# Kernel optimization log

Measured on AMD Instinct MI355X. Metric: run time of the kernel, lower is better.

Reference implementation:

```python
import jax, jax.numpy as jnp
import numpy as np
from jax import lax

WS = (8, 7, 7)
NUM_HEADS = 8
KEY_DIM = 16
D = 32  # attn_ratio * key_dim == dim // num_heads
DIM = 256
B = 128
EPS = 1e-5
SCALE = KEY_DIM ** -0.5


def _rel_index():
    d, h, w = WS
    coords = np.stack(np.meshgrid(np.arange(d), np.arange(h), np.arange(w), indexing='ij'))  # [3,d,h,w]
    cf = coords.reshape(3, -1)
    rc = (cf[:, :, None] - cf[:, None, :]).transpose(1, 2, 0)  # [N,N,3]
    rc[..., 0] += d - 1
    rc[..., 1] += h - 1
    rc[..., 2] += w - 1
    rc[..., 0] *= (2 * h - 1) * (2 * w - 1)
    rc[..., 1] *= 2 * w - 1
    return rc.sum(-1).astype(np.int32)  # [N,N]


def setup_inputs() -> dict:
    key = jax.random.key(0)
    ks = jax.random.split(key, 20)
    table = (2 * WS[0] - 1) * (2 * WS[1] - 1) * (2 * WS[2] - 1)  # 2535
    f32 = jnp.float32
    inp = {
        'x': jax.random.normal(ks[0], (B, DIM) + WS, f32),
        'qkv_w': jax.random.normal(ks[1], (NUM_HEADS, 2 * KEY_DIM + D, DIM // NUM_HEADS), f32) * 0.1,
        'qkv_g': 0.5 + 0.5 * jax.random.uniform(ks[2], (NUM_HEADS, 2 * KEY_DIM + D), f32),
        'qkv_b': jax.random.normal(ks[3], (NUM_HEADS, 2 * KEY_DIM + D), f32) * 0.1,
        'qkv_m': jax.random.normal(ks[4], (NUM_HEADS, 2 * KEY_DIM + D), f32) * 0.1,
        'qkv_v': 0.5 + jax.random.uniform(ks[5], (NUM_HEADS, 2 * KEY_DIM + D), f32),
        'dw_w': jax.random.normal(ks[6], (NUM_HEADS, KEY_DIM, 1, 3, 3, 3), f32) * 0.1,
        'dw_g': 0.5 + 0.5 * jax.random.uniform(ks[7], (NUM_HEADS, KEY_DIM), f32),
        'dw_b': jax.random.normal(ks[8], (NUM_HEADS, KEY_DIM), f32) * 0.1,
        'dw_m': jax.random.normal(ks[9], (NUM_HEADS, KEY_DIM), f32) * 0.1,
        'dw_v': 0.5 + jax.random.uniform(ks[10], (NUM_HEADS, KEY_DIM), f32),
        'proj_w': jax.random.normal(ks[11], (DIM, D * NUM_HEADS), f32) * 0.05,
        'proj_g': 0.5 + 0.5 * jax.random.uniform(ks[12], (DIM,), f32),
        'proj_b': jax.random.normal(ks[13], (DIM,), f32) * 0.1,
        'proj_m': jax.random.normal(ks[14], (DIM,), f32) * 0.1,
        'proj_v': 0.5 + jax.random.uniform(ks[15], (DIM,), f32),
        'rpb': jax.random.normal(ks[16], (table, NUM_HEADS), f32) * 0.02,
        'rel_index': jnp.asarray(_rel_index()),
    }
    return inp


def _bn(x, g, b, m, v):
    # x: [B, C, N], inference-form batchnorm over channel axis 1
    s = g / jnp.sqrt(v + EPS)
    return x * s[None, :, None] + (b - m * s)[None, :, None]


def reference(x, qkv_w, qkv_g, qkv_b, qkv_m, qkv_v, dw_w, dw_g, dw_b, dw_m, dw_v,
              proj_w, proj_g, proj_b, proj_m, proj_v, rpb, rel_index):
    Bsz, C, Wd, Wh, Ww = x.shape
    N = Wd * Wh * Ww
    nh = qkv_w.shape[0]
    # relative position bias: [nh, N, N]
    bias = rpb[rel_index.reshape(-1)].reshape(N, N, nh).transpose(2, 0, 1)
    feats_in = jnp.split(x.reshape(Bsz, C, N), nh, axis=1)  # nh x [B, C/nh, N]
    feats_out = []
    feat = feats_in[0]
    for i in range(nh):
        if i > 0:
            feat = feat + feats_in[i]
        # 1x1x1 conv + BN
        h = jnp.einsum('oi,bin->bon', qkv_w[i], feat)
        h = _bn(h, qkv_g[i], qkv_b[i], qkv_m[i], qkv_v[i])
        q, k, v = jnp.split(h, [KEY_DIM, 2 * KEY_DIM], axis=1)  # [B,kd,N],[B,kd,N],[B,d,N]
        # depthwise 3x3x3 conv on q + BN
        q3 = q.reshape(Bsz, KEY_DIM, Wd, Wh, Ww)
        q3 = lax.conv_general_dilated(q3, dw_w[i], window_strides=(1, 1, 1),
                                      padding=((1, 1), (1, 1), (1, 1)),
                                      feature_group_count=KEY_DIM,
                                      dimension_numbers=('NCDHW', 'OIDHW', 'NCDHW'))
        q = _bn(q3.reshape(Bsz, KEY_DIM, N), dw_g[i], dw_b[i], dw_m[i], dw_v[i])
        # attention over the N window tokens
        attn = jnp.einsum('bcn,bcm->bnm', q, k) * SCALE + bias[i]
        attn = jax.nn.softmax(attn, axis=-1)
        feat = jnp.einsum('bcm,bnm->bcn', v, attn)  # v @ attn^T -> [B, d, N]
        feats_out.append(feat)
    cat = jnp.concatenate(feats_out, axis=1)  # [B, d*nh, N]
    out = jnp.einsum('oi,bin->bon', proj_w, jax.nn.relu(cat))
    out = _bn(out, proj_g, proj_b, proj_m, proj_v)
    return out.reshape(Bsz, C, Wd, Wh, Ww)
```

## Files before the change

kernel.cpp:

```cpp
#include <hip/hip_runtime.h>
#include <hip/hip_bf16.h>
#include <cstdint>
#include <cstddef>


#define NH    8
#define KD    16
#define DV    32
#define CH    32
#define QKVO  64
#define DIMC  256
#define NTOK  392
#define NPAD  448
#define BSZ   128
#define EPSV  1e-5f
#define SCL2  0.3606737602222409f
#define LOG2E 1.4426950408889634f
#define MQ    98

typedef float f32x4 __attribute__((ext_vector_type(4)));
typedef short bf16x8 __attribute__((ext_vector_type(8)));
typedef unsigned int u32x4 __attribute__((ext_vector_type(4)));
typedef unsigned int u32x2 __attribute__((ext_vector_type(2)));

__device__ inline unsigned rne_bf16_bits(float x) {
  unsigned u = __float_as_uint(x);
  return (u + 0x7fffu + ((u >> 16) & 1u)) >> 16;
}
__device__ inline unsigned cvt_pk(float a, float b) {
  unsigned r;
  asm("v_cvt_pk_bf16_f32 %0, %1, %2" : "=v"(r) : "v"(a), "v"(b));
  return r;
}
__device__ inline float b2f_lo(unsigned w) { return __uint_as_float(w << 16); }
__device__ inline float b2f_hi(unsigned w) { return __uint_as_float(w & 0xffff0000u); }

__global__ __launch_bounds__(256) void k_biasM(const float* __restrict__ rpb,
                                               const int* __restrict__ rel,
                                               float* __restrict__ biasM) {
  int idx = blockIdx.x * 256 + threadIdx.x;
  if (idx >= NH * MQ * NTOK * 4) return;
  int j = idx & 3;
  int r1 = idx >> 2;
  int n = r1 % NTOK;
  int r2 = r1 / NTOK;
  int mq = r2 % MQ;
  int h = r2 / MQ;
  int m = min(4 * mq + j, NTOK - 1);
  biasM[idx] = rpb[rel[n * NTOK + m] * NH + h] * LOG2E;
}

__global__ __launch_bounds__(256) void k_wsplit(const float* __restrict__ W,
                                                short* __restrict__ Whi,
                                                short* __restrict__ Wlo) {
  int i = blockIdx.x * 256 + threadIdx.x;
  if (i >= DIMC * DIMC) return;
  float v = W[i];
  unsigned u = __float_as_uint(v) & 0xffff0000u;
  Whi[i] = (short)(u >> 16);
  Wlo[i] = (short)rne_bf16_bits(v - __uint_as_float(u));
}
__global__ __launch_bounds__(256) void k_wsplitq(const float* __restrict__ W,
                                                 short* __restrict__ Whi,
                                                 short* __restrict__ Wlo) {
  int i = blockIdx.x * 256 + threadIdx.x;
  if (i >= NH * QKVO * CH) return;
  float v = W[i];
  unsigned u = __float_as_uint(v) & 0xffff0000u;
  Whi[i] = (short)(u >> 16);
  Wlo[i] = (short)rne_bf16_bits(v - __uint_as_float(u));
}

__global__ __launch_bounds__(256) void k_qkv0(
    const float* __restrict__ x, const float* __restrict__ W,
    const float* __restrict__ G, const float* __restrict__ Bp,
    const float* __restrict__ Mp, const float* __restrict__ Vp,
    float* __restrict__ qb0, short* __restrict__ kT0, short* __restrict__ vb0,
    short* __restrict__ kT1, short* __restrict__ vb1) {
  int t = threadIdx.x;
  int b = blockIdx.y;
  int n = blockIdx.x * 64 + (t & 63);
  int w = t >> 6;
  int o0 = __builtin_amdgcn_readfirstlane(w * 16);
  int nc = min(n, NTOK - 1);

  const float* xp = x + (size_t)b * DIMC * NTOK + nc;
  float f[CH];
#pragma unroll
  for (int c = 0; c < CH; ++c) f[c] = xp[(size_t)c * NTOK];

  float acc[16];
#pragma unroll
  for (int oi = 0; oi < 16; ++oi) acc[oi] = 0.f;
#pragma unroll
  for (int c = 0; c < CH; ++c) {
    float fv = f[c];
#pragma unroll
    for (int oi = 0; oi < 16; ++oi) acc[oi] += W[(o0 + oi) * CH + c] * fv;
  }
  float r[16];
#pragma unroll
  for (int oi = 0; oi < 16; ++oi) {
    int o = o0 + oi;
    float s = G[o] * rsqrtf(Vp[o] + EPSV);
    float sh = Bp[o] - Mp[o] * s;
    r[oi] = acc[oi] * s + sh;
  }

  if (w == 0) {
    if (n < NTOK) {
#pragma unroll
      for (int oi = 0; oi < 16; ++oi)
        qb0[((size_t)b * KD + oi) * NTOK + n] = r[oi];
    }
  } else if (w == 1) {
    unsigned wh[8], wl[8];
#pragma unroll
    for (int i = 0; i < 8; ++i) wh[i] = cvt_pk(r[2 * i], r[2 * i + 1]);
#pragma unroll
    for (int i = 0; i < 8; ++i)
      wl[i] = cvt_pk(r[2 * i] - b2f_lo(wh[i]), r[2 * i + 1] - b2f_hi(wh[i]));
    short* row = kT0 + ((size_t)b * NPAD + n) * 32;
    *(u32x4*)&row[0]  = (u32x4){wh[0], wh[1], wh[2], wh[3]};
    *(u32x4*)&row[8]  = (u32x4){wh[4], wh[5], wh[6], wh[7]};
    *(u32x4*)&row[16] = (u32x4){wl[0], wl[1], wl[2], wl[3]};
    *(u32x4*)&row[24] = (u32x4){wl[4], wl[5], wl[6], wl[7]};
    if (n >= NTOK) {
      short* row1 = kT1 + ((size_t)b * NPAD + n) * 32;
#pragma unroll
      for (int p = 0; p < 4; ++p) *(u32x4*)&row1[p * 8] = (u32x4){0, 0, 0, 0};
    }
  } else {
    int vc0 = (w - 2) * 16;
#pragma unroll
    for (int oi = 0; oi < 16; ++oi)
      vb0[((size_t)b * DV + vc0 + oi) * NPAD + n] = (short)rne_bf16_bits(r[oi]);
    if (n >= NTOK) {
#pragma unroll
      for (int oi = 0; oi < 16; ++oi)
        vb1[((size_t)b * DV + vc0 + oi) * NPAD + n] = 0;
    }
  }
}

__global__ __launch_bounds__(256, 8) void k_head(int head,
    const float* __restrict__ x,
    const float* __restrict__ qbC, const short* __restrict__ kTC,
    const short* __restrict__ vbC, const float* __restrict__ biasM,
    const float* __restrict__ DW, const float* __restrict__ dG,
    const float* __restrict__ dB, const float* __restrict__ dM,
    const float* __restrict__ dV,
    const short* __restrict__ Wqhi, const short* __restrict__ Wqlo,
    const float* __restrict__ qG, const float* __restrict__ qBp,
    const float* __restrict__ qM, const float* __restrict__ qV,
    unsigned* __restrict__ catB, float* __restrict__ qbN,
    short* __restrict__ kTN, short* __restrict__ vbN) {
  __shared__ float wdw[432];
  __shared__ float qstage[16][17];
  __shared__ __align__(16) float ubuf[2304];
  __shared__ float lM[4][16];
  __shared__ float oF[32][17];
  __shared__ float xs[32][17];

  int t = threadIdx.x;
  int id = blockIdx.x;
  int r8 = id & 7;
  int jd = id >> 3;
  int qt = jd % 25;
  int b = 8 * (jd / 25) + r8;
  int w = t >> 6, l = t & 63;
  int ln = l & 15, g = l >> 4;
  int tok16 = t & 15, gr = t >> 4;
  int koff = ((g >> 1) << 4) + ((g & 1) << 3);

  {
    float (*hs)[132] = (float(*)[132])ubuf;
    for (int i = t; i < 432; i += 256) wdw[i] = DW[head * 432 + i];
    const float* qpb = qbC + (size_t)b * KD * NTOK;
    int nlo = qt * 16 - 57;
    for (int i = t; i < 16 * 130; i += 256) {
      int c = i / 130, r = i - c * 130;
      int n = nlo + r;
      hs[c][r] = (n >= 0 && n < NTOK) ? qpb[(size_t)c * NTOK + n] : 0.f;
    }
    __syncthreads();
    int tokg = qt * 16 + tok16;
    int tkc = min(tokg, NTOK - 1);
    int z = tkc / 49, rm = tkc - z * 49, y = rm / 7, xx = rm - y * 7;
    const float* wt = &wdw[gr * 27];
    float a = 0.f;
#pragma unroll
    for (int dz = 0; dz < 3; ++dz) {
      int zz = z + dz - 1;
      if (zz < 0 || zz >= 8) continue;
#pragma unroll
      for (int dy = 0; dy < 3; ++dy) {
        int yy = y + dy - 1;
        if (yy < 0 || yy >= 7) continue;
#pragma unroll
        for (int dx = 0; dx < 3; ++dx) {
          int xw = xx + dx - 1;
          if (xw < 0 || xw >= 7) continue;
          a += wt[dz * 9 + dy * 3 + dx] * hs[gr][zz * 49 + yy * 7 + xw - nlo];
        }
      }
    }
    float s = dG[head * KD + gr] * rsqrtf(dV[head * KD + gr] + EPSV);
    float sh = dB[head * KD + gr] - dM[head * KD + gr] * s;
    __syncthreads();
    qstage[gr][tok16] = (a * s + sh) * SCL2;
  }
  __syncthreads();

  bf16x8 qB1, qB2;
  {
    float qv[8];
#pragma unroll
    for (int j2 = 0; j2 < 8; ++j2) qv[j2] = qstage[8 * (g & 1) + j2][ln];
    u32x4 hw;
#pragma unroll
    for (int i = 0; i < 4; ++i) hw[i] = cvt_pk(qv[2 * i], qv[2 * i + 1]);
    qB1 = *(bf16x8*)&hw;
    if (g < 2) {
      u32x4 lw;
#pragma unroll
      for (int i = 0; i < 4; ++i)
        lw[i] = cvt_pk(qv[2 * i] - b2f_lo(hw[i]), qv[2 * i + 1] - b2f_hi(hw[i]));
      qB2 = *(bf16x8*)&lw;
    } else {
#pragma unroll
      for (int j2 = 0; j2 < 8; ++j2) qB2[j2] = 0;
    }
  }

  int tokq = qt * 16 + ln;
  int tqc = min(tokq, NTOK - 1);
  const short* kbase = kTC + (size_t)b * NPAD * 32;
  const short* vbase = vbC + (size_t)b * DV * NPAD;
  const float* bb = biasM + ((size_t)head * MQ * NTOK + tqc) * 4;
  unsigned* pb = (unsigned*)ubuf + w * 576;

  f32x4 oacc[2];
#pragma unroll
  for (int ct = 0; ct < 2; ++ct) oacc[ct] = (f32x4){0.f, 0.f, 0.f, 0.f};
  float lsum = 0.f;

  for (int mt = w; mt < 7; mt += 4) {
    int m0 = mt * 64;
    bf16x8 aK[4];
#pragma unroll
    for (int ms = 0; ms < 4; ++ms)
      aK[ms] = *(const bf16x8*)&kbase[(size_t)(m0 + 16 * ms + ln) * 32 + koff];
    f32x4 bv[4];
#pragma unroll
    for (int ms = 0; ms < 4; ++ms) {
      int mq = min((m0 + 16 * ms + 4 * g) >> 2, MQ - 1);
      bv[ms] = *(const f32x4*)&bb[(size_t)mq * (NTOK * 4)];
    }
    bf16x8 aV[4];
#pragma unroll
    for (int ch = 0; ch < 2; ++ch)
#pragma unroll
      for (int ct = 0; ct < 2; ++ct)
        aV[ch * 2 + ct] = *(const bf16x8*)&vbase[(size_t)(16 * ct + ln) * NPAD
                                                 + m0 + 32 * ch + 8 * g];
    f32x4 S[4];
#pragma unroll
    for (int ms = 0; ms < 4; ++ms) {
      f32x4 a = __builtin_amdgcn_mfma_f32_16x16x32_bf16(aK[ms], qB1, bv[ms], 0, 0, 0);
      S[ms] = __builtin_amdgcn_mfma_f32_16x16x32_bf16(aK[ms], qB2, a, 0, 0, 0);
    }
#pragma unroll
    for (int ms = 0; ms < 4; ++ms) {
      int mk = m0 + 16 * ms + 4 * g;
      float p[4];
#pragma unroll
      for (int r = 0; r < 4; ++r) {
        float sv = fminf(S[ms][r], 96.f);
        if (mk + r >= NTOK) sv = -1e30f;
        p[r] = __builtin_amdgcn_exp2f(sv);
        lsum += p[r];
      }
      u32x2 pw = (u32x2){cvt_pk(p[0], p[1]), cvt_pk(p[2], p[3])};
      *(u32x2*)&pb[ln * 36 + 8 * ms + 2 * g] = pw;
    }
#pragma unroll
    for (int ch = 0; ch < 2; ++ch) {
      u32x4 pk4 = *(const u32x4*)&pb[ln * 36 + 16 * ch + 4 * g];
      bf16x8 pf = *(bf16x8*)&pk4;
#pragma unroll
      for (int ct = 0; ct < 2; ++ct)
        oacc[ct] = __builtin_amdgcn_mfma_f32_16x16x32_bf16(aV[ch * 2 + ct], pf, oacc[ct], 0, 0, 0);
    }
  }

  __syncthreads();
  float (*oP)[32][17] = (float(*)[32][17])ubuf;
  lsum += __shfl_xor(lsum, 16);
  lsum += __shfl_xor(lsum, 32);
#pragma unroll
  for (int ct = 0; ct < 2; ++ct)
#pragma unroll
    for (int r = 0; r < 4; ++r) oP[w][16 * ct + 4 * g + r][ln] = oacc[ct][r];
  if (g == 0) lM[w][ln] = lsum;
  __syncthreads();

  {
    int tokg = qt * 16 + tok16;
    float lt = lM[0][tok16] + lM[1][tok16] + lM[2][tok16] + lM[3][tok16];
    float inv = 1.f / fmaxf(lt, 1e-30f);
    int c0 = 2 * gr, c1 = c0 + 1;
    float a0 = (oP[0][c0][tok16] + oP[1][c0][tok16] + oP[2][c0][tok16] + oP[3][c0][tok16]) * inv;
    float a1 = (oP[0][c1][tok16] + oP[1][c1][tok16] + oP[2][c1][tok16] + oP[3][c1][tok16]) * inv;
    oF[c0][tok16] = a0;
    oF[c1][tok16] = a1;
    if (tokg < NTOK)
      catB[((size_t)b * 128 + head * 16 + gr) * NTOK + tokg] =
          cvt_pk(fmaxf(a0, 0.f), fmaxf(a1, 0.f));
    if (head < 7) {
      for (int i = t; i < 512; i += 256) {
        int c = i >> 4, tk = i & 15;
        int tg = min(qt * 16 + tk, NTOK - 1);
        xs[c][tk] = x[((size_t)b * DIMC + (head + 1) * CH + c) * NTOK + tg];
      }
    }
  }
  __syncthreads();

  if (head < 7) {
    const short* wqh = Wqhi + ((size_t)(head + 1) * QKVO + 16 * w + ln) * CH + 8 * g;
    const short* wql = Wqlo + ((size_t)(head + 1) * QKVO + 16 * w + ln) * CH + 8 * g;
    bf16x8 Ah = *(const bf16x8*)wqh;
    bf16x8 Al = *(const bf16x8*)wql;
    float f8[8];
#pragma unroll
    for (int j2 = 0; j2 < 8; ++j2) f8[j2] = oF[8 * g + j2][ln] + xs[8 * g + j2][ln];
    u32x4 bh, blw;
#pragma unroll
    for (int i = 0; i < 4; ++i) {
      bh[i] = cvt_pk(f8[2 * i], f8[2 * i + 1]);
      blw[i] = cvt_pk(f8[2 * i] - b2f_lo(bh[i]), f8[2 * i + 1] - b2f_hi(bh[i]));
    }
    bf16x8 Bh = *(bf16x8*)&bh;
    bf16x8 Bl = *(bf16x8*)&blw;
    f32x4 acc = (f32x4){0.f, 0.f, 0.f, 0.f};
    acc = __builtin_amdgcn_mfma_f32_16x16x32_bf16(Ah, Bh, acc, 0, 0, 0);
    acc = __builtin_amdgcn_mfma_f32_16x16x32_bf16(Ah, Bl, acc, 0, 0, 0);
    acc = __builtin_amdgcn_mfma_f32_16x16x32_bf16(Al, Bh, acc, 0, 0, 0);
    float r4[4];
#pragma unroll
    for (int r = 0; r < 4; ++r) {
      int o = 16 * w + 4 * g + r;
      int idx = (head + 1) * QKVO + o;
      float s = qG[idx] * rsqrtf(qV[idx] + EPSV);
      float sh = qBp[idx] - qM[idx] * s;
      r4[r] = acc[r] * s + sh;
    }
    int tokg = qt * 16 + ln;
    if (tokg < NTOK) {
      if (w == 0) {
#pragma unroll
        for (int r = 0; r < 4; ++r)
          qbN[((size_t)b * KD + 4 * g + r) * NTOK + tokg] = r4[r];
      } else if (w == 1) {
        unsigned h0 = cvt_pk(r4[0], r4[1]), h1 = cvt_pk(r4[2], r4[3]);
        unsigned l0 = cvt_pk(r4[0] - b2f_lo(h0), r4[1] - b2f_hi(h0));
        unsigned l1 = cvt_pk(r4[2] - b2f_lo(h1), r4[3] - b2f_hi(h1));
        short* row = kTN + ((size_t)b * NPAD + tokg) * 32;
        *(u32x2*)&row[4 * g]      = (u32x2){h0, h1};
        *(u32x2*)&row[16 + 4 * g] = (u32x2){l0, l1};
      } else {
        int vc0 = 16 * (w - 2) + 4 * g;
#pragma unroll
        for (int r = 0; r < 4; ++r)
          vbN[((size_t)b * DV + vc0 + r) * NPAD + tokg] = (short)rne_bf16_bits(r4[r]);
      }
    }
  }
}

__global__ __launch_bounds__(256, 2) void k_proj5(const unsigned* __restrict__ catB,
    const short* __restrict__ Whi, const short* __restrict__ Wlo,
    const float* __restrict__ G, const float* __restrict__ Bp,
    const float* __restrict__ Mp, const float* __restrict__ Vp,
    float* __restrict__ out) {
  int t = threadIdx.x;
  int nt = blockIdx.x, b = blockIdx.y;
  int w = t >> 6, l = t & 63;
  int ln = l & 15, g = l >> 4;
  int n0 = nt * 64;
  int ntk[4];
#pragma unroll
  for (int ns = 0; ns < 4; ++ns) ntk[ns] = min(n0 + 16 * ns + ln, NTOK - 1);
  const unsigned* xb = catB + (size_t)b * 128 * NTOK;

  f32x4 acc[4][4];
#pragma unroll
  for (int i = 0; i < 4; ++i)
#pragma unroll
    for (int j = 0; j < 4; ++j) acc[i][j] = (f32x4){0.f, 0.f, 0.f, 0.f};

  unsigned rb[4][4];
  bf16x8 wh[4], wl[4];
  {
#pragma unroll
    for (int ns = 0; ns < 4; ++ns)
#pragma unroll
      for (int i = 0; i < 4; ++i)
        rb[ns][i] = xb[(size_t)(4 * g + i) * NTOK + ntk[ns]];
#pragma unroll
    for (int ot = 0; ot < 4; ++ot) {
      size_t wo = (size_t)(64 * w + 16 * ot + ln) * DIMC + 8 * g;
      wh[ot] = *(const bf16x8*)&Whi[wo];
      wl[ot] = *(const bf16x8*)&Wlo[wo];
    }
  }

#pragma unroll 1
  for (int c8 = 0; c8 < 8; ++c8) {
    unsigned rbn[4][4];
    bf16x8 whn[4], wln[4];
    {
      int cpn = ((c8 + 1) & 7) * 16 + 4 * g;
#pragma unroll
      for (int ns = 0; ns < 4; ++ns)
#pragma unroll
        for (int i = 0; i < 4; ++i)
          rbn[ns][i] = xb[(size_t)(cpn + i) * NTOK + ntk[ns]];
      int cwn = ((c8 + 1) & 7) * 32 + 8 * g;
#pragma unroll
      for (int ot = 0; ot < 4; ++ot) {
        size_t wo = (size_t)(64 * w + 16 * ot + ln) * DIMC + cwn;
        whn[ot] = *(const bf16x8*)&Whi[wo];
        wln[ot] = *(const bf16x8*)&Wlo[wo];
      }
    }
#pragma unroll
    for (int ns = 0; ns < 4; ++ns) {
      u32x4 bw = (u32x4){rb[ns][0], rb[ns][1], rb[ns][2], rb[ns][3]};
      bf16x8 Bf = *(bf16x8*)&bw;
#pragma unroll
      for (int ot = 0; ot < 4; ++ot) {
        acc[ot][ns] = __builtin_amdgcn_mfma_f32_16x16x32_bf16(wh[ot], Bf, acc[ot][ns], 0, 0, 0);
        acc[ot][ns] = __builtin_amdgcn_mfma_f32_16x16x32_bf16(wl[ot], Bf, acc[ot][ns], 0, 0, 0);
      }
    }
#pragma unroll
    for (int ns = 0; ns < 4; ++ns)
#pragma unroll
      for (int i = 0; i < 4; ++i) rb[ns][i] = rbn[ns][i];
#pragma unroll
    for (int ot = 0; ot < 4; ++ot) { wh[ot] = whn[ot]; wl[ot] = wln[ot]; }
  }

#pragma unroll
  for (int ot = 0; ot < 4; ++ot)
#pragma unroll
    for (int r = 0; r < 4; ++r) {
      int o = 64 * w + 16 * ot + 4 * g + r;
      float s = G[o] * rsqrtf(Vp[o] + EPSV);
      float sh = Bp[o] - Mp[o] * s;
#pragma unroll
      for (int ns = 0; ns < 4; ++ns) {
        int n = n0 + 16 * ns + ln;
        if (n < NTOK)
          out[((size_t)b * DIMC + o) * NTOK + n] = acc[ot][ns][r] * s + sh;
      }
    }
}

extern "C" void kernel_launch(void* const* d_in, const int* in_sizes, int n_in,
                              void* d_out, int out_size, void* d_ws, size_t ws_size,
                              hipStream_t stream) {
  const float* x      = (const float*)d_in[0];
  const float* qkv_w  = (const float*)d_in[1];
  const float* qkv_g  = (const float*)d_in[2];
  const float* qkv_b  = (const float*)d_in[3];
  const float* qkv_m  = (const float*)d_in[4];
  const float* qkv_v  = (const float*)d_in[5];
  const float* dw_w   = (const float*)d_in[6];
  const float* dw_g   = (const float*)d_in[7];
  const float* dw_b   = (const float*)d_in[8];
  const float* dw_m   = (const float*)d_in[9];
  const float* dw_v   = (const float*)d_in[10];
  const float* proj_w = (const float*)d_in[11];
  const float* proj_g = (const float*)d_in[12];
  const float* proj_b = (const float*)d_in[13];
  const float* proj_m = (const float*)d_in[14];
  const float* proj_v = (const float*)d_in[15];
  const float* rpb    = (const float*)d_in[16];
  const int*   rel    = (const int*)d_in[17];
  float* out = (float*)d_out;

  float* wsf  = (float*)d_ws;
  float*    biasM = wsf;
  float*    qb0  = biasM + (size_t)NH * MQ * NTOK * 4;
  float*    qb1  = qb0 + (size_t)BSZ * KD * NTOK;
  short*    kT0  = (short*)(qb1 + (size_t)BSZ * KD * NTOK);
  short*    kT1  = kT0 + (size_t)BSZ * NPAD * 32;
  short*    vb0  = kT1 + (size_t)BSZ * NPAD * 32;
  short*    vb1  = vb0 + (size_t)BSZ * DV * NPAD;
  unsigned* catB = (unsigned*)(vb1 + (size_t)BSZ * DV * NPAD);
  short*    Whi  = (short*)(catB + (size_t)BSZ * 128 * NTOK);
  short*    Wlo  = Whi + (size_t)DIMC * DIMC;
  short*    Wqhi = Wlo + (size_t)DIMC * DIMC;
  short*    Wqlo = Wqhi + (size_t)NH * QKVO * CH;

  k_biasM<<<dim3((NH * MQ * NTOK * 4 + 255) / 256), 256, 0, stream>>>(rpb, rel, biasM);
  k_wsplit<<<dim3((DIMC * DIMC + 255) / 256), 256, 0, stream>>>(proj_w, Whi, Wlo);
  k_wsplitq<<<dim3((NH * QKVO * CH + 255) / 256), 256, 0, stream>>>(qkv_w, Wqhi, Wqlo);
  k_qkv0<<<dim3(7, 128), 256, 0, stream>>>(x, qkv_w, qkv_g, qkv_b, qkv_m, qkv_v,
                                           qb0, kT0, vb0, kT1, vb1);

  for (int h = 0; h < NH; ++h) {
    float* qbC = (h & 1) ? qb1 : qb0;
    short* kTC = (h & 1) ? kT1 : kT0;
    short* vbC = (h & 1) ? vb1 : vb0;
    float* qbN = (h & 1) ? qb0 : qb1;
    short* kTN = (h & 1) ? kT0 : kT1;
    short* vbN = (h & 1) ? vb0 : vb1;
    k_head<<<dim3(3200), 256, 0, stream>>>(h, x, qbC, kTC, vbC, biasM,
        dw_w, dw_g, dw_b, dw_m, dw_v,
        Wqhi, Wqlo, qkv_g, qkv_b, qkv_m, qkv_v,
        catB, qbN, kTN, vbN);
  }

  k_proj5<<<dim3(7, 128), 256, 0, stream>>>(catB, Whi, Wlo, proj_g, proj_b,
                                            proj_m, proj_v, out);
}
```

Baseline: 366.5 us.

## Give each wave its own 16-query tile over all keys in k_head

k_head now handles 64 query tokens per block (896 blocks instead of 3200). Each wave owns 16 queries and loops over all 7 key tiles, where before the four waves split the key tiles for the same 16 queries. This removes the cross-wave LDS reduction of partial outputs and softmax sums, plus the barriers around it, and reuses the depthwise-conv halo and the x tile across more tokens. In exchange each wave reads all K and V tiles, there are fewer blocks per head launch, and occupancy drops from 8 to 4 waves per SIMD because of larger shared buffers.

```diff
diff --git a/kernel.cpp b/kernel.cpp
--- a/kernel.cpp
+++ b/kernel.cpp
@@ -143,7 +143,7 @@
   }
 }
 
-__global__ __launch_bounds__(256, 8) void k_head(int head,
+__global__ __launch_bounds__(256, 4) void k_head(int head,
     const float* __restrict__ x,
     const float* __restrict__ qbC, const short* __restrict__ kTC,
     const short* __restrict__ vbC, const float* __restrict__ biasM,
@@ -156,67 +156,77 @@
     unsigned* __restrict__ catB, float* __restrict__ qbN,
     short* __restrict__ kTN, short* __restrict__ vbN) {
   __shared__ float wdw[432];
-  __shared__ float qstage[16][17];
-  __shared__ __align__(16) float ubuf[2304];
-  __shared__ float lM[4][16];
-  __shared__ float oF[32][17];
-  __shared__ float xs[32][17];
+  __shared__ __align__(16) float ubuf[2880];
+  __shared__ float qstage[16][68];
+  __shared__ float xs[32][68];
+  __shared__ float oF[4][32][17];
 
   int t = threadIdx.x;
   int id = blockIdx.x;
   int r8 = id & 7;
   int jd = id >> 3;
-  int qt = jd % 25;
-  int b = 8 * (jd / 25) + r8;
+  int qt = jd % 7;
+  int b = 8 * (jd / 7) + r8;
+  int n0 = qt * 64;
   int w = t >> 6, l = t & 63;
   int ln = l & 15, g = l >> 4;
-  int tok16 = t & 15, gr = t >> 4;
   int koff = ((g >> 1) << 4) + ((g & 1) << 3);
 
   {
-    float (*hs)[132] = (float(*)[132])ubuf;
+    float (*hs)[180] = (float(*)[180])ubuf;
     for (int i = t; i < 432; i += 256) wdw[i] = DW[head * 432 + i];
+    if (head < 7) {
+      for (int i = t; i < 32 * 64; i += 256) {
+        int c = i >> 6, tk = i & 63;
+        xs[c][tk] = x[((size_t)b * DIMC + (head + 1) * CH + c) * NTOK
+                      + min(n0 + tk, NTOK - 1)];
+      }
+    }
     const float* qpb = qbC + (size_t)b * KD * NTOK;
-    int nlo = qt * 16 - 57;
-    for (int i = t; i < 16 * 130; i += 256) {
-      int c = i / 130, r = i - c * 130;
+    int nlo = n0 - 57;
+    for (int i = t; i < 16 * 178; i += 256) {
+      int c = i / 178, r = i - c * 178;
       int n = nlo + r;
       hs[c][r] = (n >= 0 && n < NTOK) ? qpb[(size_t)c * NTOK + n] : 0.f;
     }
     __syncthreads();
-    int tokg = qt * 16 + tok16;
-    int tkc = min(tokg, NTOK - 1);
-    int z = tkc / 49, rm = tkc - z * 49, y = rm / 7, xx = rm - y * 7;
-    const float* wt = &wdw[gr * 27];
-    float a = 0.f;
-#pragma unroll
-    for (int dz = 0; dz < 3; ++dz) {
-      int zz = z + dz - 1;
-      if (zz < 0 || zz >= 8) continue;
-#pragma unroll
-      for (int dy = 0; dy < 3; ++dy) {
-        int yy = y + dy - 1;
-        if (yy < 0 || yy >= 7) continue;
-#pragma unroll
-        for (int dx = 0; dx < 3; ++dx) {
-          int xw = xx + dx - 1;
-          if (xw < 0 || xw >= 7) continue;
-          a += wt[dz * 9 + dy * 3 + dx] * hs[gr][zz * 49 + yy * 7 + xw - nlo];
+    int c = t >> 4;
+    float s = dG[head * KD + c] * rsqrtf(dV[head * KD + c] + EPSV);
+    float sh = dB[head * KD + c] - dM[head * KD + c] * s;
+    const float* wt = &wdw[c * 27];
+#pragma unroll
+    for (int tt = 0; tt < 4; ++tt) {
+      int tl = (t & 15) + 16 * tt;
+      int tkc = min(n0 + tl, NTOK - 1);
+      int z = tkc / 49, rm = tkc - z * 49, y = rm / 7, xx = rm - y * 7;
+      float a = 0.f;
+#pragma unroll
+      for (int dz = 0; dz < 3; ++dz) {
+        int zz = z + dz - 1;
+        if (zz < 0 || zz >= 8) continue;
+#pragma unroll
+        for (int dy = 0; dy < 3; ++dy) {
+          int yy = y + dy - 1;
+          if (yy < 0 || yy >= 7) continue;
+#pragma unroll
+          for (int dx = 0; dx < 3; ++dx) {
+            int xw = xx + dx - 1;
+            if (xw < 0 || xw >= 7) continue;
+            a += wt[dz * 9 + dy * 3 + dx] * hs[c][zz * 49 + yy * 7 + xw - nlo];
+          }
         }
       }
-    }
-    float s = dG[head * KD + gr] * rsqrtf(dV[head * KD + gr] + EPSV);
-    float sh = dB[head * KD + gr] - dM[head * KD + gr] * s;
-    __syncthreads();
-    qstage[gr][tok16] = (a * s + sh) * SCL2;
+      qstage[c][tl] = (a * s + sh) * SCL2;
+    }
   }
   __syncthreads();
 
+  int tl0 = 16 * w + ln;
   bf16x8 qB1, qB2;
   {
     float qv[8];
 #pragma unroll
-    for (int j2 = 0; j2 < 8; ++j2) qv[j2] = qstage[8 * (g & 1) + j2][ln];
+    for (int j2 = 0; j2 < 8; ++j2) qv[j2] = qstage[8 * (g & 1) + j2][tl0];
     u32x4 hw;
 #pragma unroll
     for (int i = 0; i < 4; ++i) hw[i] = cvt_pk(qv[2 * i], qv[2 * i + 1]);
@@ -233,19 +243,20 @@
     }
   }
 
-  int tokq = qt * 16 + ln;
+  int tokq = n0 + tl0;
   int tqc = min(tokq, NTOK - 1);
   const short* kbase = kTC + (size_t)b * NPAD * 32;
   const short* vbase = vbC + (size_t)b * DV * NPAD;
   const float* bb = biasM + ((size_t)head * MQ * NTOK + tqc) * 4;
-  unsigned* pb = (unsigned*)ubuf + w * 576;
+  unsigned* pb = (unsigned*)ubuf + w * 720;
 
   f32x4 oacc[2];
 #pragma unroll
   for (int ct = 0; ct < 2; ++ct) oacc[ct] = (f32x4){0.f, 0.f, 0.f, 0.f};
   float lsum = 0.f;
 
-  for (int mt = w; mt < 7; mt += 4) {
+#pragma unroll 1
+  for (int mt = 0; mt < 7; ++mt) {
     int m0 = mt * 64;
     bf16x8 aK[4];
 #pragma unroll
@@ -294,47 +305,31 @@
     }
   }
 
-  __syncthreads();
-  float (*oP)[32][17] = (float(*)[32][17])ubuf;
   lsum += __shfl_xor(lsum, 16);
   lsum += __shfl_xor(lsum, 32);
-#pragma unroll
-  for (int ct = 0; ct < 2; ++ct)
-#pragma unroll
-    for (int r = 0; r < 4; ++r) oP[w][16 * ct + 4 * g + r][ln] = oacc[ct][r];
-  if (g == 0) lM[w][ln] = lsum;
-  __syncthreads();
-
-  {
-    int tokg = qt * 16 + tok16;
-    float lt = lM[0][tok16] + lM[1][tok16] + lM[2][tok16] + lM[3][tok16];
-    float inv = 1.f / fmaxf(lt, 1e-30f);
-    int c0 = 2 * gr, c1 = c0 + 1;
-    float a0 = (oP[0][c0][tok16] + oP[1][c0][tok16] + oP[2][c0][tok16] + oP[3][c0][tok16]) * inv;
-    float a1 = (oP[0][c1][tok16] + oP[1][c1][tok16] + oP[2][c1][tok16] + oP[3][c1][tok16]) * inv;
-    oF[c0][tok16] = a0;
-    oF[c1][tok16] = a1;
-    if (tokg < NTOK)
-      catB[((size_t)b * 128 + head * 16 + gr) * NTOK + tokg] =
-          cvt_pk(fmaxf(a0, 0.f), fmaxf(a1, 0.f));
-    if (head < 7) {
-      for (int i = t; i < 512; i += 256) {
-        int c = i >> 4, tk = i & 15;
-        int tg = min(qt * 16 + tk, NTOK - 1);
-        xs[c][tk] = x[((size_t)b * DIMC + (head + 1) * CH + c) * NTOK + tg];
-      }
-    }
-  }
-  __syncthreads();
+  float inv = 1.f / fmaxf(lsum, 1e-30f);
+#pragma unroll
+  for (int ct = 0; ct < 2; ++ct) {
+    float o0v = oacc[ct][0] * inv, o1v = oacc[ct][1] * inv;
+    float o2v = oacc[ct][2] * inv, o3v = oacc[ct][3] * inv;
+    oF[w][16 * ct + 4 * g + 0][ln] = o0v;
+    oF[w][16 * ct + 4 * g + 1][ln] = o1v;
+    oF[w][16 * ct + 4 * g + 2][ln] = o2v;
+    oF[w][16 * ct + 4 * g + 3][ln] = o3v;
+    if (tokq < NTOK) {
+      int p0 = head * 16 + 8 * ct + 2 * g;
+      catB[((size_t)b * 128 + p0) * NTOK + tokq] =
+          cvt_pk(fmaxf(o0v, 0.f), fmaxf(o1v, 0.f));
+      catB[((size_t)b * 128 + p0 + 1) * NTOK + tokq] =
+          cvt_pk(fmaxf(o2v, 0.f), fmaxf(o3v, 0.f));
+    }
+  }
 
   if (head < 7) {
-    const short* wqh = Wqhi + ((size_t)(head + 1) * QKVO + 16 * w + ln) * CH + 8 * g;
-    const short* wql = Wqlo + ((size_t)(head + 1) * QKVO + 16 * w + ln) * CH + 8 * g;
-    bf16x8 Ah = *(const bf16x8*)wqh;
-    bf16x8 Al = *(const bf16x8*)wql;
     float f8[8];
 #pragma unroll
-    for (int j2 = 0; j2 < 8; ++j2) f8[j2] = oF[8 * g + j2][ln] + xs[8 * g + j2][ln];
+    for (int j2 = 0; j2 < 8; ++j2)
+      f8[j2] = oF[w][8 * g + j2][ln] + xs[8 * g + j2][tl0];
     u32x4 bh, blw;
 #pragma unroll
     for (int i = 0; i < 4; ++i) {
@@ -343,37 +338,41 @@
     }
     bf16x8 Bh = *(bf16x8*)&bh;
     bf16x8 Bl = *(bf16x8*)&blw;
-    f32x4 acc = (f32x4){0.f, 0.f, 0.f, 0.f};
-    acc = __builtin_amdgcn_mfma_f32_16x16x32_bf16(Ah, Bh, acc, 0, 0, 0);
-    acc = __builtin_amdgcn_mfma_f32_16x16x32_bf16(Ah, Bl, acc, 0, 0, 0);
-    acc = __builtin_amdgcn_mfma_f32_16x16x32_bf16(Al, Bh, acc, 0, 0, 0);
-    float r4[4];
-#pragma unroll
-    for (int r = 0; r < 4; ++r) {
-      int o = 16 * w + 4 * g + r;
-      int idx = (head + 1) * QKVO + o;
-      float s = qG[idx] * rsqrtf(qV[idx] + EPSV);
-      float sh = qBp[idx] - qM[idx] * s;
-      r4[r] = acc[r] * s + sh;
-    }
-    int tokg = qt * 16 + ln;
-    if (tokg < NTOK) {
-      if (w == 0) {
-#pragma unroll
-        for (int r = 0; r < 4; ++r)
-          qbN[((size_t)b * KD + 4 * g + r) * NTOK + tokg] = r4[r];
-      } else if (w == 1) {
-        unsigned h0 = cvt_pk(r4[0], r4[1]), h1 = cvt_pk(r4[2], r4[3]);
-        unsigned l0 = cvt_pk(r4[0] - b2f_lo(h0), r4[1] - b2f_hi(h0));
-        unsigned l1 = cvt_pk(r4[2] - b2f_lo(h1), r4[3] - b2f_hi(h1));
-        short* row = kTN + ((size_t)b * NPAD + tokg) * 32;
-        *(u32x2*)&row[4 * g]      = (u32x2){h0, h1};
-        *(u32x2*)&row[16 + 4 * g] = (u32x2){l0, l1};
-      } else {
-        int vc0 = 16 * (w - 2) + 4 * g;
-#pragma unroll
-        for (int r = 0; r < 4; ++r)
-          vbN[((size_t)b * DV + vc0 + r) * NPAD + tokg] = (short)rne_bf16_bits(r4[r]);
+#pragma unroll
+    for (int ot = 0; ot < 4; ++ot) {
+      size_t wo = ((size_t)(head + 1) * QKVO + 16 * ot + ln) * CH + 8 * g;
+      bf16x8 Ah = *(const bf16x8*)&Wqhi[wo];
+      bf16x8 Al = *(const bf16x8*)&Wqlo[wo];
+      f32x4 acc = (f32x4){0.f, 0.f, 0.f, 0.f};
+      acc = __builtin_amdgcn_mfma_f32_16x16x32_bf16(Ah, Bh, acc, 0, 0, 0);
+      acc = __builtin_amdgcn_mfma_f32_16x16x32_bf16(Ah, Bl, acc, 0, 0, 0);
+      acc = __builtin_amdgcn_mfma_f32_16x16x32_bf16(Al, Bh, acc, 0, 0, 0);
+      float r4[4];
+#pragma unroll
+      for (int r = 0; r < 4; ++r) {
+        int idx = (head + 1) * QKVO + 16 * ot + 4 * g + r;
+        float s = qG[idx] * rsqrtf(qV[idx] + EPSV);
+        float sh = qBp[idx] - qM[idx] * s;
+        r4[r] = acc[r] * s + sh;
+      }
+      if (tokq < NTOK) {
+        if (ot == 0) {
+#pragma unroll
+          for (int r = 0; r < 4; ++r)
+            qbN[((size_t)b * KD + 4 * g + r) * NTOK + tokq] = r4[r];
+        } else if (ot == 1) {
+          unsigned h0 = cvt_pk(r4[0], r4[1]), h1 = cvt_pk(r4[2], r4[3]);
+          unsigned l0 = cvt_pk(r4[0] - b2f_lo(h0), r4[1] - b2f_hi(h0));
+          unsigned l1 = cvt_pk(r4[2] - b2f_lo(h1), r4[3] - b2f_hi(h1));
+          short* row = kTN + ((size_t)b * NPAD + tokq) * 32;
+          *(u32x2*)&row[4 * g]      = (u32x2){h0, h1};
+          *(u32x2*)&row[16 + 4 * g] = (u32x2){l0, l1};
+        } else {
+          int vc0 = 16 * (ot - 2) + 4 * g;
+#pragma unroll
+          for (int r = 0; r < 4; ++r)
+            vbN[((size_t)b * DV + vc0 + r) * NPAD + tokq] = (short)rne_bf16_bits(r4[r]);
+        }
       }
     }
   }
@@ -519,7 +518,7 @@
     float* qbN = (h & 1) ? qb0 : qb1;
     short* kTN = (h & 1) ? kT0 : kT1;
     short* vbN = (h & 1) ? vb0 : vb1;
-    k_head<<<dim3(3200), 256, 0, stream>>>(h, x, qbC, kTC, vbC, biasM,
+    k_head<<<dim3(896), 256, 0, stream>>>(h, x, qbC, kTC, vbC, biasM,
         dw_w, dw_g, dw_b, dw_m, dw_v,
         Wqhi, Wqlo, qkv_g, qkv_b, qkv_m, qkv_v,
         catB, qbN, kTN, vbN);
```

After: 402.0 us. 1.1x slower.
